# Performance work log

Hardware: AMD Instinct MI355X
Metric: run time of the kernel (lower is better)

## Reference

```python
import jax, jax.numpy as jnp
import numpy as np

N = 8192
NHID = 256

def setup_inputs() -> dict:
    key = jax.random.key(0)
    ks = jax.random.split(key, 9)
    s = 1.0 / np.sqrt(NHID)  # torch Linear default init scale
    return {
        "x1": jax.random.normal(ks[0], (N, NHID), jnp.float32),
        "x2": jax.random.normal(ks[1], (N, NHID), jnp.float32),
        "x3": jax.random.normal(ks[2], (N, NHID), jnp.float32),
        "Wq": jax.random.uniform(ks[3], (NHID, NHID), jnp.float32, -s, s),
        "bq": jax.random.uniform(ks[4], (NHID,), jnp.float32, -s, s),
        "Wk": jax.random.uniform(ks[5], (NHID, NHID), jnp.float32, -s, s),
        "bk": jax.random.uniform(ks[6], (NHID,), jnp.float32, -s, s),
        "Wv": jax.random.uniform(ks[7], (NHID, NHID), jnp.float32, -s, s),
        "bv": jax.random.uniform(ks[8], (NHID,), jnp.float32, -s, s),
    }

def reference(x1, x2, x3, Wq, bq, Wk, bk, Wv, bv):
    # torch.nn.Linear: y = x @ W.T + b
    q = x1 @ Wq.T + bq                      # [N, nhid]
    k = x2 @ Wk.T + bk                      # [N, nhid]
    v = x3 @ Wv.T + bv                      # [N, nhid]
    scores = q @ k.T                        # [N, N], NOTE: unscaled (no 1/sqrt(d))
    attn = jax.nn.softmax(scores, axis=1)   # softmax over keys (dim=1)
    return attn @ v                         # [N, nhid]
```

## Files before the change

kernel.cpp:

```cpp
#include <hip/hip_runtime.h>
#include <stdint.h>

typedef unsigned short u16;
typedef __attribute__((ext_vector_type(8))) short short8;
typedef __attribute__((ext_vector_type(4))) float f32x4;
typedef __attribute__((ext_vector_type(16))) float f32x16;

#define LOG2E 1.4426950408889634f
#define NT 8192
#define DH 256

#define QH     0
#define KH     2097152
#define VTB    4194304
#define OPARTB 6291456
#define XH0 6291456
#define XL0 8388608
#define XH1 10485760
#define XL1 12582912
#define XH2 14680064
#define XL2 16777216
#define WQH 18874368
#define WQL 18939904
#define WKH 19005440
#define WKL 19070976
#define WVH 19136512
#define WVL 19202048
#define MPART_F 11534336
#define LPART_F 11599872

__device__ __forceinline__ u16 f2bf(float f) {
  union { float f; uint32_t u; } c; c.f = f;
  uint32_t u = c.u;
  return (u16)((u + 0x7fffu + ((u >> 16) & 1)) >> 16);
}
__device__ __forceinline__ float bf2f(u16 h) {
  union { uint32_t u; float f; } c; c.u = ((uint32_t)h) << 16;
  return c.f;
}

__device__ __forceinline__ int swz32(int u, int h) {
  return (u & 24) | ((u & 7) ^ (h & 7));
}

__device__ __forceinline__ f32x4 mfma16(short8 a, short8 b, f32x4 c) {
  return __builtin_amdgcn_mfma_f32_16x16x32_bf16(a, b, c, 0, 0, 0);
}
__device__ __forceinline__ f32x16 mfma32(short8 a, short8 b, f32x16 c) {
  return __builtin_amdgcn_mfma_f32_32x32x16_bf16(a, b, c, 0, 0, 0);
}

__device__ __forceinline__ void gl_lds16(const u16* g, u16* l) {
  __builtin_amdgcn_global_load_lds(
      (const __attribute__((address_space(1))) uint32_t*)g,
      (__attribute__((address_space(3))) uint32_t*)l, 16, 0, 0);
}

__global__ __launch_bounds__(256) void k_convert(
    const float* __restrict__ x1, const float* __restrict__ x2, const float* __restrict__ x3,
    const float* __restrict__ wq, const float* __restrict__ wk, const float* __restrict__ wv,
    u16* __restrict__ wsu) {
  int b = blockIdx.x;
  const float* src; u16 *dh, *dl; int bl;
  if (b < 1024)      { src = x1; dh = wsu + XH0; dl = wsu + XL0; bl = b; }
  else if (b < 2048) { src = x2; dh = wsu + XH1; dl = wsu + XL1; bl = b - 1024; }
  else if (b < 3072) { src = x3; dh = wsu + XH2; dl = wsu + XL2; bl = b - 2048; }
  else if (b < 3104) { src = wq; dh = wsu + WQH; dl = wsu + WQL; bl = b - 3072; }
  else if (b < 3136) { src = wk; dh = wsu + WKH; dl = wsu + WKL; bl = b - 3104; }
  else               { src = wv; dh = wsu + WVH; dl = wsu + WVL; bl = b - 3136; }
  int i = (bl * 256 + threadIdx.x) * 8;
  f32x4 a = *(const f32x4*)(src + i);
  f32x4 c = *(const f32x4*)(src + i + 4);
  short8 rh, rl;
  float v[8] = {a[0], a[1], a[2], a[3], c[0], c[1], c[2], c[3]};
#pragma unroll
  for (int j = 0; j < 8; j++) {
    u16 h = f2bf(v[j]);
    rh[j] = (short)h;
    rl[j] = (short)f2bf(v[j] - bf2f(h));
  }
  *(short8*)(dh + i) = rh;
  *(short8*)(dl + i) = rl;
}

__global__ __launch_bounds__(256) void k_qkv(
    u16* __restrict__ wsu,
    const float* __restrict__ bq, const float* __restrict__ bk, const float* __restrict__ bv) {
  __shared__ u16 sAh[32 * 256];
  __shared__ u16 sAl[32 * 256];
  __shared__ u16 sBh[32 * 256];
  __shared__ u16 sBl[32 * 256];
  int bx = blockIdx.x;
  int mid = bx >> 8;
  int t = bx & 255;
  const u16 *Ah, *Al, *Bh, *Bl; u16 *O; const float* bias;
  int rowA0, colBase, ldO, biasRow;
  if (mid == 0) {
    Ah = wsu + XH0; Al = wsu + XL0; Bh = wsu + WQH; Bl = wsu + WQL;
    O = wsu + QH; bias = bq; biasRow = 0; ldO = 256;
    rowA0 = t * 32; colBase = 0;
  } else if (mid == 1) {
    Ah = wsu + XH1; Al = wsu + XL1; Bh = wsu + WKH; Bl = wsu + WKL;
    O = wsu + KH; bias = bk; biasRow = 0; ldO = 256;
    rowA0 = t * 32; colBase = 0;
  } else {
    Ah = wsu + WVH; Al = wsu + WVL; Bh = wsu + XH2; Bl = wsu + XL2;
    O = wsu + VTB; bias = bv; biasRow = 1; ldO = 8192;
    rowA0 = (t & 7) * 32; colBase = (t >> 3) * 256;
  }

  int tid = threadIdx.x;
  int lane = tid & 63, wave = tid >> 6;
  int n = lane & 15, quad = lane >> 4;
  int wm = wave >> 1, wn = wave & 1;

#pragma unroll
  for (int i = 0; i < 4; i++) {
    int L = i * 256 + tid;
    int row = L >> 5, u = L & 31;
    short8 vh = *(const short8*)(Ah + (size_t)(rowA0 + row) * 256 + u * 8);
    short8 vl = *(const short8*)(Al + (size_t)(rowA0 + row) * 256 + u * 8);
    *(short8*)(&sAh[row * 256 + swz32(u, row) * 8]) = vh;
    *(short8*)(&sAl[row * 256 + swz32(u, row) * 8]) = vl;
  }

  int brow0 = wave * 2 + (lane >> 5);
  int bgu = (lane & 24) | ((lane & 7) ^ (brow0 & 7));

#pragma unroll
  for (int i = 0; i < 4; i++) {
    gl_lds16(Bh + (size_t)(colBase + i * 8 + brow0) * 256 + bgu * 8, &sBh[i * 2048 + wave * 512]);
    gl_lds16(Bl + (size_t)(colBase + i * 8 + brow0) * 256 + bgu * 8, &sBl[i * 2048 + wave * 512]);
  }

#pragma unroll 1
  for (int g = 0; g < 8; g++) {
    __syncthreads();

    int colg = colBase + g * 32 + wn * 16 + n;
    f32x4 acc = {0.f, 0.f, 0.f, 0.f};
#pragma unroll
    for (int kk = 0; kk < 8; kk++) {
      int ra = wm * 16 + n;
      int rbB = wn * 16 + n;
      short8 ah = *(const short8*)(&sAh[ra * 256 + swz32(kk * 4 + quad, ra) * 8]);
      short8 al = *(const short8*)(&sAl[ra * 256 + swz32(kk * 4 + quad, ra) * 8]);
      short8 bh = *(const short8*)(&sBh[rbB * 256 + swz32(kk * 4 + quad, rbB) * 8]);
      short8 bl = *(const short8*)(&sBl[rbB * 256 + swz32(kk * 4 + quad, rbB) * 8]);
      acc = mfma16(ah, bh, acc);
      acc = mfma16(ah, bl, acc);
      acc = mfma16(al, bh, acc);
    }

    if (g < 7) {
      __syncthreads();
      int b0 = colBase + (g + 1) * 32;
#pragma unroll
      for (int i = 0; i < 4; i++) {
        gl_lds16(Bh + (size_t)(b0 + i * 8 + brow0) * 256 + bgu * 8, &sBh[i * 2048 + wave * 512]);
        gl_lds16(Bl + (size_t)(b0 + i * 8 + brow0) * 256 + bgu * 8, &sBl[i * 2048 + wave * 512]);
      }
    }

    float bcol = biasRow ? 0.0f : bias[colg];
#pragma unroll
    for (int r = 0; r < 4; r++) {
      int rowg = rowA0 + wm * 16 + quad * 4 + r;
      float bb = biasRow ? bias[rowg] : bcol;
      O[(size_t)rowg * ldO + colg] = f2bf(acc[r] + bb);
    }
  }
}

__global__ __launch_bounds__(256, 2) void k_flash(
    const u16* __restrict__ wsu, u16* __restrict__ opart, float* __restrict__ wsf) {
  __shared__ u16 smem[32768];

  int qb = blockIdx.x >> 3, sp = blockIdx.x & 7;
  int tid = threadIdx.x, lane = tid & 63, wave = tid >> 6;
  int key = lane & 31;
  int h = lane >> 5;
  const u16* Qp = wsu + QH;
  const u16* Kp = wsu + KH;
  const u16* Vp = wsu + VTB;

  int rowQ0 = qb * 128 + wave * 32;

  short8 qf[16];
#pragma unroll
  for (int kk = 0; kk < 16; kk++)
    qf[kk] = *(const short8*)(Qp + (size_t)(rowQ0 + key) * 256 + kk * 16 + h * 8);

  int koff[4];
#pragma unroll
  for (int m = 0; m < 4; m++)
    koff[m] = key * 512 + 16 * ((2 * m + h) ^ (key & 7));
  int voff[2];
#pragma unroll
  for (int c = 0; c < 2; c++)
    voff[c] = key * 64 + 16 * ((2 * c + h) ^ ((key >> 1) & 3));

  int krow0 = wave * 2 + h;
  int kgu = (lane & 24) | ((lane & 7) ^ (krow0 & 7));
  int vd_base = wave * 16 + (lane >> 2);
  int vgu = (lane & 3) ^ ((lane >> 3) & 3);

  int key00 = sp * 1024;

#pragma unroll
  for (int i = 0; i < 4; i++) {
    gl_lds16(Kp + (size_t)(key00 + i * 8 + krow0) * 256 + kgu * 8,
             &smem[i * 2048 + wave * 512]);
  }

  f32x16 o[8];
#pragma unroll
  for (int dt = 0; dt < 8; dt++)
#pragma unroll
    for (int r = 0; r < 16; r++) o[dt][r] = 0.f;
  float negm0 = 0.f, lcur = 0.f;

  union PB { uint32_t u[4]; short8 s8; };
  PB pb0, pb1;
#pragma unroll
  for (int j = 0; j < 4; j++) { pb0.u[j] = 0u; pb1.u[j] = 0u; }

#pragma unroll 1
  for (int it = 0; it < 32; it++) {
    __syncthreads();
    int cur = it & 1;
    const u16* sKc = &smem[cur * 8192];
    if (it + 1 < 32) {
      int k1 = key00 + (it + 1) * 32;
#pragma unroll
      for (int i = 0; i < 4; i++)
        gl_lds16(Kp + (size_t)(k1 + i * 8 + krow0) * 256 + kgu * 8,
                 &smem[(cur ^ 1) * 8192 + i * 2048 + wave * 512]);
    }
    {
      int kv = key00 + it * 32;
#pragma unroll
      for (int i = 0; i < 4; i++)
        gl_lds16(Vp + (size_t)(i * 64 + vd_base) * 8192 + kv + vgu * 8,
                 &smem[16384 + cur * 8192 + i * 2048 + wave * 512]);
    }

    const u16* sVp = (it > 0) ? &smem[16384 + (cur ^ 1) * 8192] : sKc;

    f32x16 s;
#pragma unroll
    for (int r = 0; r < 16; r++) s[r] = 0.f;
    __builtin_amdgcn_s_setprio(1);
#pragma unroll
    for (int kk = 0; kk < 16; kk++) {
      short8 kf = *(const short8*)((const char*)sKc + koff[kk & 3] + 128 * (kk >> 2));
      s = mfma32(kf, qf[kk], s);
    }
#pragma unroll
    for (int dt = 0; dt < 8; dt++) {
      short8 v0 = *(const short8*)((const char*)sVp + voff[0] + dt * 2048);
      o[dt] = mfma32(v0, pb0.s8, o[dt]);
    }
#pragma unroll
    for (int dt = 0; dt < 8; dt++) {
      short8 v1 = *(const short8*)((const char*)sVp + voff[1] + dt * 2048);
      o[dt] = mfma32(v1, pb1.s8, o[dt]);
    }
    __builtin_amdgcn_s_setprio(0);

    if (it == 0) {
      float mv = s[0];
#pragma unroll
      for (int r = 1; r < 16; r++) mv = fmaxf(mv, s[r]);
      mv = fmaxf(mv, __shfl_xor(mv, 32));
      negm0 = -mv * LOG2E;
    }

    uint32_t c8[8];
#pragma unroll
    for (int j = 0; j < 8; j++) {
      float x0 = fminf(fmaf(s[2 * j],     LOG2E, negm0), 110.f);
      float x1 = fminf(fmaf(s[2 * j + 1], LOG2E, negm0), 110.f);
      float p0 = exp2f(x0);
      float p1 = exp2f(x1);
      lcur += p0 + p1;
      asm("v_cvt_pk_bf16_f32 %0, %1, %2" : "=v"(c8[j]) : "v"(p0), "v"(p1));
    }
    uint32_t w0a = c8[0], w2a = c8[2], w1a = c8[1], w3a = c8[3];
    asm("v_permlane32_swap_b32 %0, %1" : "+v"(w0a), "+v"(w2a));
    asm("v_permlane32_swap_b32 %0, %1" : "+v"(w1a), "+v"(w3a));
    uint32_t w0b = c8[4], w2b = c8[6], w1b = c8[5], w3b = c8[7];
    asm("v_permlane32_swap_b32 %0, %1" : "+v"(w0b), "+v"(w2b));
    asm("v_permlane32_swap_b32 %0, %1" : "+v"(w1b), "+v"(w3b));
    pb0.u[0] = w0a; pb0.u[1] = w1a; pb0.u[2] = w2a; pb0.u[3] = w3a;
    pb1.u[0] = w0b; pb1.u[1] = w1b; pb1.u[2] = w2b; pb1.u[3] = w3b;
  }

  __syncthreads();
  {
    const u16* sVp = &smem[16384 + 8192];
    __builtin_amdgcn_s_setprio(1);
#pragma unroll
    for (int dt = 0; dt < 8; dt++) {
      short8 v0 = *(const short8*)((const char*)sVp + voff[0] + dt * 2048);
      o[dt] = mfma32(v0, pb0.s8, o[dt]);
    }
#pragma unroll
    for (int dt = 0; dt < 8; dt++) {
      short8 v1 = *(const short8*)((const char*)sVp + voff[1] + dt * 2048);
      o[dt] = mfma32(v1, pb1.s8, o[dt]);
    }
    __builtin_amdgcn_s_setprio(0);
  }

  lcur += __shfl_xor(lcur, 32);

  __syncthreads();
  u16* tb = &smem[wave * 8192];
#pragma unroll
  for (int dt = 0; dt < 8; dt++)
#pragma unroll
    for (int j = 0; j < 4; j++) {
      uint32_t a, b;
      asm("v_cvt_pk_bf16_f32 %0, %1, %2" : "=v"(a) : "v"(o[dt][4 * j + 0]), "v"(o[dt][4 * j + 1]));
      asm("v_cvt_pk_bf16_f32 %0, %1, %2" : "=v"(b) : "v"(o[dt][4 * j + 2]), "v"(o[dt][4 * j + 3]));
      int u16i = (dt * 4 + j) ^ (key & 7);
      uint2 val; val.x = a; val.y = b;
      *(uint2*)((char*)tb + key * 512 + u16i * 16 + h * 8) = val;
    }
  u16* op = opart + (size_t)sp * (NT * DH);
#pragma unroll
  for (int c2i = 0; c2i < 16; c2i++) {
    int rl = c2i * 2 + h;
    int uu = lane & 31;
    short8 vv = *(const short8*)((const char*)tb + rl * 512 + ((uu ^ (rl & 7)) * 16));
    *(short8*)(op + (size_t)(rowQ0 + rl) * 256 + uu * 8) = vv;
  }

  if (lane < 32) {
    int row = rowQ0 + key;
    wsf[MPART_F + sp * NT + row] = negm0 * -0.6931471805599453f;
    wsf[LPART_F + sp * NT + row] = lcur;
  }
}

__global__ __launch_bounds__(256) void k_combine(
    const u16* __restrict__ opart, const float* __restrict__ wsf, float* __restrict__ out) {
  int gid = blockIdx.x * 256 + threadIdx.x;
  int row = gid >> 6, cg = gid & 63;
  float m[8], l[8];
#pragma unroll
  for (int s = 0; s < 8; s++) {
    m[s] = wsf[MPART_F + s * NT + row];
    l[s] = wsf[LPART_F + s * NT + row];
  }
  float ms = m[0];
#pragma unroll
  for (int s = 1; s < 8; s++) ms = fmaxf(ms, m[s]);
  float denom = 0.f;
  float acc[4] = {0.f, 0.f, 0.f, 0.f};
#pragma unroll
  for (int s = 0; s < 8; s++) {
    float w = exp2f((m[s] - ms) * LOG2E);
    denom += w * l[s];
    const u16* pp = opart + ((size_t)s * NT + row) * 256 + cg * 4;
    uint2 v = *(const uint2*)pp;
    acc[0] += w * bf2f((u16)(v.x & 0xffff));
    acc[1] += w * bf2f((u16)(v.x >> 16));
    acc[2] += w * bf2f((u16)(v.y & 0xffff));
    acc[3] += w * bf2f((u16)(v.y >> 16));
  }
  float inv = 1.0f / denom;
  f32x4 r = {acc[0] * inv, acc[1] * inv, acc[2] * inv, acc[3] * inv};
  *(f32x4*)(out + (size_t)row * 256 + cg * 4) = r;
}

extern "C" void kernel_launch(void* const* d_in, const int* in_sizes, int n_in,
                              void* d_out, int out_size, void* d_ws, size_t ws_size,
                              hipStream_t stream) {
  const float* x1 = (const float*)d_in[0];
  const float* x2 = (const float*)d_in[1];
  const float* x3 = (const float*)d_in[2];
  const float* Wq = (const float*)d_in[3];
  const float* bq = (const float*)d_in[4];
  const float* Wk = (const float*)d_in[5];
  const float* bk = (const float*)d_in[6];
  const float* Wv = (const float*)d_in[7];
  const float* bv = (const float*)d_in[8];
  u16* wsu = (u16*)d_ws;
  float* wsf = (float*)d_ws;
  float* out = (float*)d_out;

  k_convert<<<dim3(3168), dim3(256), 0, stream>>>(x1, x2, x3, Wq, Wk, Wv, wsu);
  k_qkv<<<dim3(768), dim3(256), 0, stream>>>(wsu, bq, bk, bv);
  k_flash<<<dim3(512), dim3(256), 0, stream>>>(wsu, wsu + OPARTB, wsf);
  k_combine<<<dim3(2048), dim3(256), 0, stream>>>(wsu + OPARTB, wsf, out);
}
```

Measured before the change: 207.1 us.

## Fuse fp32-to-bf16 split conversion into QKV projection kernel

```diff
diff --git a/kernel.cpp b/kernel.cpp
--- a/kernel.cpp
+++ b/kernel.cpp
@@ -14,18 +14,6 @@
 #define KH     2097152
 #define VTB    4194304
 #define OPARTB 6291456
-#define XH0 6291456
-#define XL0 8388608
-#define XH1 10485760
-#define XL1 12582912
-#define XH2 14680064
-#define XL2 16777216
-#define WQH 18874368
-#define WQL 18939904
-#define WKH 19005440
-#define WKL 19070976
-#define WVH 19136512
-#define WVL 19202048
 #define MPART_F 11534336
 #define LPART_F 11599872
 
@@ -56,118 +44,123 @@
       (__attribute__((address_space(3))) uint32_t*)l, 16, 0, 0);
 }
 
-__global__ __launch_bounds__(256) void k_convert(
+__device__ __forceinline__ void cvt8(const float* v, short8& vh, short8& vl) {
+#pragma unroll
+  for (int j = 0; j < 8; j++) {
+    u16 hh = f2bf(v[j]);
+    vh[j] = (short)hh;
+    vl[j] = (short)f2bf(v[j] - bf2f(hh));
+  }
+}
+
+__global__ __launch_bounds__(256) void k_qkv2(
     const float* __restrict__ x1, const float* __restrict__ x2, const float* __restrict__ x3,
-    const float* __restrict__ wq, const float* __restrict__ wk, const float* __restrict__ wv,
+    const float* __restrict__ wqp, const float* __restrict__ bqp,
+    const float* __restrict__ wkp, const float* __restrict__ bkp,
+    const float* __restrict__ wvp, const float* __restrict__ bvp,
     u16* __restrict__ wsu) {
-  int b = blockIdx.x;
-  const float* src; u16 *dh, *dl; int bl;
-  if (b < 1024)      { src = x1; dh = wsu + XH0; dl = wsu + XL0; bl = b; }
-  else if (b < 2048) { src = x2; dh = wsu + XH1; dl = wsu + XL1; bl = b - 1024; }
-  else if (b < 3072) { src = x3; dh = wsu + XH2; dl = wsu + XL2; bl = b - 2048; }
-  else if (b < 3104) { src = wq; dh = wsu + WQH; dl = wsu + WQL; bl = b - 3072; }
-  else if (b < 3136) { src = wk; dh = wsu + WKH; dl = wsu + WKL; bl = b - 3104; }
-  else               { src = wv; dh = wsu + WVH; dl = wsu + WVL; bl = b - 3136; }
-  int i = (bl * 256 + threadIdx.x) * 8;
-  f32x4 a = *(const f32x4*)(src + i);
-  f32x4 c = *(const f32x4*)(src + i + 4);
-  short8 rh, rl;
-  float v[8] = {a[0], a[1], a[2], a[3], c[0], c[1], c[2], c[3]};
-#pragma unroll
-  for (int j = 0; j < 8; j++) {
-    u16 h = f2bf(v[j]);
-    rh[j] = (short)h;
-    rl[j] = (short)f2bf(v[j] - bf2f(h));
-  }
-  *(short8*)(dh + i) = rh;
-  *(short8*)(dl + i) = rl;
-}
-
-__global__ __launch_bounds__(256) void k_qkv(
-    u16* __restrict__ wsu,
-    const float* __restrict__ bq, const float* __restrict__ bk, const float* __restrict__ bv) {
-  __shared__ u16 sAh[32 * 256];
-  __shared__ u16 sAl[32 * 256];
-  __shared__ u16 sBh[32 * 256];
-  __shared__ u16 sBl[32 * 256];
-  int bx = blockIdx.x;
-  int mid = bx >> 8;
-  int t = bx & 255;
-  const u16 *Ah, *Al, *Bh, *Bl; u16 *O; const float* bias;
-  int rowA0, colBase, ldO, biasRow;
-  if (mid == 0) {
-    Ah = wsu + XH0; Al = wsu + XL0; Bh = wsu + WQH; Bl = wsu + WQL;
-    O = wsu + QH; bias = bq; biasRow = 0; ldO = 256;
-    rowA0 = t * 32; colBase = 0;
-  } else if (mid == 1) {
-    Ah = wsu + XH1; Al = wsu + XL1; Bh = wsu + WKH; Bl = wsu + WKL;
-    O = wsu + KH; bias = bk; biasRow = 0; ldO = 256;
-    rowA0 = t * 32; colBase = 0;
-  } else {
-    Ah = wsu + WVH; Al = wsu + WVL; Bh = wsu + XH2; Bl = wsu + XL2;
-    O = wsu + VTB; bias = bv; biasRow = 1; ldO = 8192;
-    rowA0 = (t & 7) * 32; colBase = (t >> 3) * 256;
-  }
-
-  int tid = threadIdx.x;
+  __shared__ u16 smem[32768];
+  u16* sAh = smem;
+  u16* sAl = smem + 8192;
+  u16* sBh = smem + 16384;
+  u16* sBl = smem + 24576;
+
+  int bid = blockIdx.x, tid = threadIdx.x;
   int lane = tid & 63, wave = tid >> 6;
   int n = lane & 15, quad = lane >> 4;
   int wm = wave >> 1, wn = wave & 1;
 
-#pragma unroll
-  for (int i = 0; i < 4; i++) {
-    int L = i * 256 + tid;
-    int row = L >> 5, u = L & 31;
-    short8 vh = *(const short8*)(Ah + (size_t)(rowA0 + row) * 256 + u * 8);
-    short8 vl = *(const short8*)(Al + (size_t)(rowA0 + row) * 256 + u * 8);
-    *(short8*)(&sAh[row * 256 + swz32(u, row) * 8]) = vh;
-    *(short8*)(&sAl[row * 256 + swz32(u, row) * 8]) = vl;
-  }
-
-  int brow0 = wave * 2 + (lane >> 5);
-  int bgu = (lane & 24) | ((lane & 7) ^ (brow0 & 7));
-
-#pragma unroll
-  for (int i = 0; i < 4; i++) {
-    gl_lds16(Bh + (size_t)(colBase + i * 8 + brow0) * 256 + bgu * 8, &sBh[i * 2048 + wave * 512]);
-    gl_lds16(Bl + (size_t)(colBase + i * 8 + brow0) * 256 + bgu * 8, &sBl[i * 2048 + wave * 512]);
-  }
-
 #pragma unroll 1
-  for (int g = 0; g < 8; g++) {
+  for (int item = 0; item < 2; item++) {
+    const float *Asrc, *Bsrc, *bias; u16* O;
+    int rowA0, colBase, ldO, biasRow, nG;
+    if (item == 0) {
+      if (bid < 256) { Asrc = x1; Bsrc = wqp; bias = bqp; O = wsu + QH; rowA0 = bid * 32; }
+      else           { Asrc = x2; Bsrc = wkp; bias = bkp; O = wsu + KH; rowA0 = (bid - 256) * 32; }
+      colBase = 0; ldO = 256; biasRow = 0; nG = 8;
+    } else {
+      Asrc = wvp; Bsrc = x3; bias = bvp; O = wsu + VTB;
+      rowA0 = (bid & 7) * 32; colBase = (bid >> 3) * 128; ldO = 8192; biasRow = 1; nG = 4;
+    }
+
     __syncthreads();
 
-    int colg = colBase + g * 32 + wn * 16 + n;
-    f32x4 acc = {0.f, 0.f, 0.f, 0.f};
-#pragma unroll
-    for (int kk = 0; kk < 8; kk++) {
-      int ra = wm * 16 + n;
-      int rbB = wn * 16 + n;
-      short8 ah = *(const short8*)(&sAh[ra * 256 + swz32(kk * 4 + quad, ra) * 8]);
-      short8 al = *(const short8*)(&sAl[ra * 256 + swz32(kk * 4 + quad, ra) * 8]);
-      short8 bh = *(const short8*)(&sBh[rbB * 256 + swz32(kk * 4 + quad, rbB) * 8]);
-      short8 bl = *(const short8*)(&sBl[rbB * 256 + swz32(kk * 4 + quad, rbB) * 8]);
-      acc = mfma16(ah, bh, acc);
-      acc = mfma16(ah, bl, acc);
-      acc = mfma16(al, bh, acc);
-    }
-
-    if (g < 7) {
+#pragma unroll
+    for (int i = 0; i < 4; i++) {
+      int L = i * 256 + tid, row = L >> 5, u = L & 31;
+      const float* p = Asrc + (size_t)(rowA0 + row) * 256 + u * 8;
+      f32x4 a = *(const f32x4*)p, c = *(const f32x4*)(p + 4);
+      float v[8] = {a[0], a[1], a[2], a[3], c[0], c[1], c[2], c[3]};
+      short8 vh, vl; cvt8(v, vh, vl);
+      *(short8*)(&sAh[row * 256 + swz32(u, row) * 8]) = vh;
+      *(short8*)(&sAl[row * 256 + swz32(u, row) * 8]) = vl;
+    }
+
+    f32x4 pf[8];
+#pragma unroll
+    for (int i = 0; i < 4; i++) {
+      int L = i * 256 + tid, row = L >> 5, u = L & 31;
+      const float* p = Bsrc + (size_t)(colBase + row) * 256 + u * 8;
+      pf[i * 2] = *(const f32x4*)p; pf[i * 2 + 1] = *(const f32x4*)(p + 4);
+    }
+#pragma unroll
+    for (int i = 0; i < 4; i++) {
+      int L = i * 256 + tid, row = L >> 5, u = L & 31;
+      float v[8] = {pf[i*2][0], pf[i*2][1], pf[i*2][2], pf[i*2][3],
+                    pf[i*2+1][0], pf[i*2+1][1], pf[i*2+1][2], pf[i*2+1][3]};
+      short8 vh, vl; cvt8(v, vh, vl);
+      *(short8*)(&sBh[row * 256 + swz32(u, row) * 8]) = vh;
+      *(short8*)(&sBl[row * 256 + swz32(u, row) * 8]) = vl;
+    }
+
+#pragma unroll 1
+    for (int g = 0; g < nG; g++) {
       __syncthreads();
-      int b0 = colBase + (g + 1) * 32;
-#pragma unroll
-      for (int i = 0; i < 4; i++) {
-        gl_lds16(Bh + (size_t)(b0 + i * 8 + brow0) * 256 + bgu * 8, &sBh[i * 2048 + wave * 512]);
-        gl_lds16(Bl + (size_t)(b0 + i * 8 + brow0) * 256 + bgu * 8, &sBl[i * 2048 + wave * 512]);
+
+      if (g + 1 < nG) {
+        int b0 = colBase + (g + 1) * 32;
+#pragma unroll
+        for (int i = 0; i < 4; i++) {
+          int L = i * 256 + tid, row = L >> 5, u = L & 31;
+          const float* p = Bsrc + (size_t)(b0 + row) * 256 + u * 8;
+          pf[i * 2] = *(const f32x4*)p; pf[i * 2 + 1] = *(const f32x4*)(p + 4);
+        }
       }
-    }
-
-    float bcol = biasRow ? 0.0f : bias[colg];
-#pragma unroll
-    for (int r = 0; r < 4; r++) {
-      int rowg = rowA0 + wm * 16 + quad * 4 + r;
-      float bb = biasRow ? bias[rowg] : bcol;
-      O[(size_t)rowg * ldO + colg] = f2bf(acc[r] + bb);
+
+      int colg = colBase + g * 32 + wn * 16 + n;
+      f32x4 acc = {0.f, 0.f, 0.f, 0.f};
+#pragma unroll
+      for (int kk = 0; kk < 8; kk++) {
+        int ra = wm * 16 + n, rbB = wn * 16 + n;
+        short8 ah = *(const short8*)(&sAh[ra * 256 + swz32(kk * 4 + quad, ra) * 8]);
+        short8 al = *(const short8*)(&sAl[ra * 256 + swz32(kk * 4 + quad, ra) * 8]);
+        short8 bh = *(const short8*)(&sBh[rbB * 256 + swz32(kk * 4 + quad, rbB) * 8]);
+        short8 bl = *(const short8*)(&sBl[rbB * 256 + swz32(kk * 4 + quad, rbB) * 8]);
+        acc = mfma16(ah, bh, acc);
+        acc = mfma16(ah, bl, acc);
+        acc = mfma16(al, bh, acc);
+      }
+
+      __syncthreads();
+      if (g + 1 < nG) {
+#pragma unroll
+        for (int i = 0; i < 4; i++) {
+          int L = i * 256 + tid, row = L >> 5, u = L & 31;
+          float v[8] = {pf[i*2][0], pf[i*2][1], pf[i*2][2], pf[i*2][3],
+                        pf[i*2+1][0], pf[i*2+1][1], pf[i*2+1][2], pf[i*2+1][3]};
+          short8 vh, vl; cvt8(v, vh, vl);
+          *(short8*)(&sBh[row * 256 + swz32(u, row) * 8]) = vh;
+          *(short8*)(&sBl[row * 256 + swz32(u, row) * 8]) = vl;
+        }
+      }
+
+      float bcol = biasRow ? 0.0f : bias[colg];
+#pragma unroll
+      for (int r = 0; r < 4; r++) {
+        int rowg = rowA0 + wm * 16 + quad * 4 + r;
+        float bb = biasRow ? bias[rowg] : bcol;
+        O[(size_t)rowg * ldO + colg] = f2bf(acc[r] + bb);
+      }
     }
   }
 }
@@ -391,8 +384,7 @@
   float* wsf = (float*)d_ws;
   float* out = (float*)d_out;
 
-  k_convert<<<dim3(3168), dim3(256), 0, stream>>>(x1, x2, x3, Wq, Wk, Wv, wsu);
-  k_qkv<<<dim3(768), dim3(256), 0, stream>>>(wsu, bq, bk, bv);
+  k_qkv2<<<dim3(512), dim3(256), 0, stream>>>(x1, x2, x3, Wq, bq, Wk, bk, Wv, bv, wsu);
   k_flash<<<dim3(512), dim3(256), 0, stream>>>(wsu, wsu + OPARTB, wsf);
   k_combine<<<dim3(2048), dim3(256), 0, stream>>>(wsu + OPARTB, wsf, out);
 }
```

After: 196.9 us (median of 2 runs). 1.05x faster.
